# Performance work log

Hardware: AMD Instinct MI355X
Metric: run time of the kernel (lower is better)

The kernel has to match this reference:

```python
import jax, jax.numpy as jnp
import numpy as np

EPS = 1e-06

def phi(x):
    # canonical linear-attention feature map: elu(x) + 1 (positive features)
    return jax.nn.elu(x) + 1.0

def setup_inputs() -> dict:
    key = jax.random.key(0)
    kq, kk, kv = jax.random.split(key, 3)
    B, H, S, D = 4, 16, 4096, 64
    query = jax.random.normal(kq, (B, H, S, D), dtype=jnp.float32)
    k = jax.random.normal(kk, (B, H, S, D), dtype=jnp.float32)
    value = jax.random.normal(kv, (B, H, S, D), dtype=jnp.float32)
    attention_mask = jnp.ones((B, S), dtype=jnp.float32)
    return {"query": query, "key": k, "value": value, "attention_mask": attention_mask}

def reference(query, key, value, attention_mask):
    B, H, S, D = query.shape
    q = query / jnp.sqrt(jnp.asarray(D, query.dtype))
    phi_q = phi(q)                                   # [b,h,n,d]
    phi_k = phi(key)                                 # [b,h,n,d]
    mask = attention_mask[:, None, :, None].astype(phi_k.dtype)  # [b,1,n,1]
    phi_k = phi_k * mask
    kv_term = jnp.einsum('bhnd,bhnv->bhdv', phi_k, value)        # [b,h,d,v]
    output = jnp.einsum('bhnd,bhdv->bhnv', phi_q, kv_term)       # [b,h,n,v]
    k_one = jnp.sum(phi_k, axis=2)                               # [b,h,d] == phi_k @ masked ones
    normalizer = jnp.einsum('bhnd,bhd->bhn', phi_q, k_one)[..., None]  # [b,h,n,1]
    return output / (normalizer + EPS)
```

## Files before the change

### kernel.cpp

```cpp
#include <hip/hip_runtime.h>

typedef unsigned short ushort_t;
typedef unsigned int uint32;
typedef __bf16 bf16x8 __attribute__((ext_vector_type(8)));
typedef float f32x4 __attribute__((ext_vector_type(4)));

#define NB 4
#define NH 16
#define NS 4096
#define ND 64
#define NBH 64
#define EPSF 1e-6f

#define CH1 16
#define ROWS1 (NS / CH1)
#define P2R 64
#define LDJ 70
#define LDJW 35
#define BTSZ (80 * 64)

__device__ __forceinline__ float phi_f(float x) {
    return x > 0.0f ? x + 1.0f : __expf(x);
}
__device__ __forceinline__ ushort_t bf16_rn(float x) {
    uint32 u = __float_as_uint(x);
    uint32 r = (u + 0x7FFFu + ((u >> 16) & 1u)) >> 16;
    return (ushort_t)r;
}
__device__ __forceinline__ void split2(float x, ushort_t& h, ushort_t& l) {
    h = bf16_rn(x);
    float hf = __uint_as_float(((uint32)h) << 16);
    l = bf16_rn(x - hf);
}
union FragU { uint32 u[4]; bf16x8 v; };
__device__ __forceinline__ bf16x8 ld_frag(const ushort_t* arr, int widx) {
    const uint32* p = (const uint32*)arr;
    FragU f;
    f.u[0] = p[widx]; f.u[1] = p[widx + 1]; f.u[2] = p[widx + 2]; f.u[3] = p[widx + 3];
    return f.v;
}
union FragP { ushort_t s[8]; bf16x8 v; };
__device__ __forceinline__ f32x4 mfma16(bf16x8 a, bf16x8 b, f32x4 c) {
    return __builtin_amdgcn_mfma_f32_16x16x32_bf16(a, b, c, 0, 0, 0);
}

template<bool PART>
__global__ __launch_bounds__(256, 4)
void la_pass1(const float* __restrict__ Kin, const float* __restrict__ Vin,
              const float* __restrict__ Min, float* __restrict__ okv,
              float* __restrict__ ok1)
{
    const int t  = threadIdx.x;
    const int cx = blockIdx.x;
    const int bh = blockIdx.y;
    const int bb = bh >> 4;
    const float* Kb = Kin + (long long)bh * NS * ND;
    const float* Vb = Vin + (long long)bh * NS * ND;
    const float* Mb = Min + (long long)bb * NS;

    __shared__ __align__(16) ushort_t skh[64 * LDJ], skl[64 * LDJ];
    __shared__ __align__(16) ushort_t svh[64 * LDJ], svl[64 * LDJ];

    const int rr0 = t >> 4;
    const int c   = (t & 15) * 4;
    const int wv  = t >> 6;
    const int m   = t & 15;
    const int q   = (t & 63) >> 4;

    const f32x4 zf = {0.f, 0.f, 0.f, 0.f};
    f32x4 acc0 = zf, acc1 = zf, acc2 = zf, acc3 = zf;
    float k1loc[4] = {0.f, 0.f, 0.f, 0.f};

    const int s0 = cx * ROWS1;

    float4 kR[2][4], vR[2][4];
    float  mR[2][4];
#define LOADT(tt, sset) { \
        const long long rb_ = (long long)(s0 + (tt) * 64 + rr0); \
        const float* kp_ = Kb + rb_ * ND + c; \
        const float* vp_ = Vb + rb_ * ND + c; \
        kR[sset][0] = *(const float4*)(kp_);            vR[sset][0] = *(const float4*)(vp_); \
        kR[sset][1] = *(const float4*)(kp_ + 16 * ND);  vR[sset][1] = *(const float4*)(vp_ + 16 * ND); \
        kR[sset][2] = *(const float4*)(kp_ + 32 * ND);  vR[sset][2] = *(const float4*)(vp_ + 32 * ND); \
        kR[sset][3] = *(const float4*)(kp_ + 48 * ND);  vR[sset][3] = *(const float4*)(vp_ + 48 * ND); \
        mR[sset][0] = Mb[rb_];      mR[sset][1] = Mb[rb_ + 16]; \
        mR[sset][2] = Mb[rb_ + 32]; mR[sset][3] = Mb[rb_ + 48]; }

    LOADT(0, 0);
    __builtin_amdgcn_sched_barrier(0);

    #pragma unroll
    for (int tile = 0; tile < ROWS1 / 64; ++tile) {
        const int cur = tile & 1;
        const int nxt = cur ^ 1;
        if (tile + 1 < ROWS1 / 64) {
            LOADT(tile + 1, nxt);
            __builtin_amdgcn_sched_barrier(0);
        }
        __syncthreads();
        #pragma unroll
        for (int j = 0; j < 4; ++j) {
            const int rr = rr0 + 16 * j;
            const float xs[4] = {kR[cur][j].x, kR[cur][j].y, kR[cur][j].z, kR[cur][j].w};
            const float vs[4] = {vR[cur][j].x, vR[cur][j].y, vR[cur][j].z, vR[cur][j].w};
            const float mj = mR[cur][j];
            #pragma unroll
            for (int i = 0; i < 4; ++i) {
                const float x = phi_f(xs[i]) * mj;
                k1loc[i] += x;
                ushort_t h, l;
                split2(x, h, l);
                skh[(c + i) * LDJ + rr] = h;
                skl[(c + i) * LDJ + rr] = l;
                split2(vs[i], h, l);
                svh[(c + i) * LDJ + rr] = h;
                svl[(c + i) * LDJ + rr] = l;
            }
        }
        __syncthreads();
        #pragma unroll
        for (int ks = 0; ks < 2; ++ks) {
            const int fo = ks * 16 + q * 4;
            const bf16x8 ah = ld_frag(skh, (16 * wv + m) * LDJW + fo);
            const bf16x8 al = ld_frag(skl, (16 * wv + m) * LDJW + fo);
            {
                const bf16x8 fbh = ld_frag(svh, (0 + m) * LDJW + fo);
                const bf16x8 fbl = ld_frag(svl, (0 + m) * LDJW + fo);
                acc0 = mfma16(al, fbh, acc0); acc0 = mfma16(ah, fbl, acc0); acc0 = mfma16(ah, fbh, acc0);
            }
            {
                const bf16x8 fbh = ld_frag(svh, (16 + m) * LDJW + fo);
                const bf16x8 fbl = ld_frag(svl, (16 + m) * LDJW + fo);
                acc1 = mfma16(al, fbh, acc1); acc1 = mfma16(ah, fbl, acc1); acc1 = mfma16(ah, fbh, acc1);
            }
            {
                const bf16x8 fbh = ld_frag(svh, (32 + m) * LDJW + fo);
                const bf16x8 fbl = ld_frag(svl, (32 + m) * LDJW + fo);
                acc2 = mfma16(al, fbh, acc2); acc2 = mfma16(ah, fbl, acc2); acc2 = mfma16(ah, fbh, acc2);
            }
            {
                const bf16x8 fbh = ld_frag(svh, (48 + m) * LDJW + fo);
                const bf16x8 fbl = ld_frag(svl, (48 + m) * LDJW + fo);
                acc3 = mfma16(al, fbh, acc3); acc3 = mfma16(ah, fbl, acc3); acc3 = mfma16(ah, fbh, acc3);
            }
        }
    }
#undef LOADT

    const int dbase = 16 * wv + q * 4;
    if (PART) {
        float* outp = okv + (long long)(bh * CH1 + cx) * (ND * ND);
        #pragma unroll
        for (int i = 0; i < 4; ++i) {
            outp[(dbase + i) * ND +  0 + m] = acc0[i];
            outp[(dbase + i) * ND + 16 + m] = acc1[i];
            outp[(dbase + i) * ND + 32 + m] = acc2[i];
            outp[(dbase + i) * ND + 48 + m] = acc3[i];
        }
    } else {
        float* outp = okv + (long long)bh * (ND * ND);
        #pragma unroll
        for (int i = 0; i < 4; ++i) {
            atomicAdd(&outp[(dbase + i) * ND +  0 + m], acc0[i]);
            atomicAdd(&outp[(dbase + i) * ND + 16 + m], acc1[i]);
            atomicAdd(&outp[(dbase + i) * ND + 32 + m], acc2[i]);
            atomicAdd(&outp[(dbase + i) * ND + 48 + m], acc3[i]);
        }
    }
    __syncthreads();
    float* red = (float*)skh;
    #pragma unroll
    for (int i = 0; i < 4; ++i) red[(c + i) * 17 + rr0] = k1loc[i];
    __syncthreads();
    if (t < 64) {
        float s = 0.f;
        #pragma unroll
        for (int g = 0; g < 16; ++g) s += red[t * 17 + g];
        if (PART) ok1[(bh * CH1 + cx) * ND + t] = s;
        else      atomicAdd(&ok1[bh * ND + t], s);
    }
}

__global__ __launch_bounds__(256)
void la_reduce(const float* __restrict__ pkv, const float* __restrict__ pk1,
               ushort_t* __restrict__ BTh, ushort_t* __restrict__ BTl)
{
    const int t = threadIdx.x;
    const int bh = blockIdx.x;
    const float4* src = (const float4*)(pkv + (long long)bh * CH1 * ND * ND);
    float4 a[4];
    #pragma unroll
    for (int i = 0; i < 4; ++i) { a[i].x = 0.f; a[i].y = 0.f; a[i].z = 0.f; a[i].w = 0.f; }
    for (int c = 0; c < CH1; ++c) {
        #pragma unroll
        for (int i = 0; i < 4; ++i) {
            const float4 v = src[c * 1024 + t + 256 * i];
            a[i].x += v.x; a[i].y += v.y; a[i].z += v.z; a[i].w += v.w;
        }
    }
    ushort_t* oh = BTh + (long long)bh * BTSZ;
    ushort_t* ol = BTl + (long long)bh * BTSZ;
    #pragma unroll
    for (int i = 0; i < 4; ++i) {
        const int e4 = t + 256 * i;
        const int d  = e4 >> 4;
        const int v0 = (e4 & 15) * 4;
        const float vals[4] = {a[i].x, a[i].y, a[i].z, a[i].w};
        #pragma unroll
        for (int j = 0; j < 4; ++j) {
            ushort_t h, l; split2(vals[j], h, l);
            oh[(v0 + j) * ND + d] = h;
            ol[(v0 + j) * ND + d] = l;
        }
    }
    if (t < ND) {
        float s = 0.f;
        for (int c = 0; c < CH1; ++c) s += pk1[(bh * CH1 + c) * ND + t];
        ushort_t h, l; split2(s, h, l);
        oh[64 * ND + t] = h; ol[64 * ND + t] = l;
    }
    for (int z = t; z < 15 * 64; z += 256) { oh[65 * ND + z] = 0; ol[65 * ND + z] = 0; }
}

__global__ __launch_bounds__(256)
void la_convert(const float* __restrict__ kv, const float* __restrict__ k1,
                ushort_t* __restrict__ BTh, ushort_t* __restrict__ BTl)
{
    const int t = threadIdx.x;
    const int bh = blockIdx.x;
    const float* kvb = kv + (long long)bh * ND * ND;
    ushort_t* oh = BTh + (long long)bh * BTSZ;
    ushort_t* ol = BTl + (long long)bh * BTSZ;
    for (int e = t; e < ND * ND; e += 256) {
        const int d = e >> 6, v = e & 63;
        ushort_t h, l; split2(kvb[e], h, l);
        oh[v * ND + d] = h; ol[v * ND + d] = l;
    }
    if (t < ND) { ushort_t h, l; split2(k1[bh * ND + t], h, l); oh[64 * ND + t] = h; ol[64 * ND + t] = l; }
    for (int z = t; z < 15 * 64; z += 256) { oh[65 * ND + z] = 0; ol[65 * ND + z] = 0; }
}

__global__ __launch_bounds__(256, 2)
void la_pass2(const float* __restrict__ Qin, const ushort_t* __restrict__ BTh,
              const ushort_t* __restrict__ BTl, float* __restrict__ Out)
{
    const int t  = threadIdx.x;
    const int bh = blockIdx.y;
    const int s0 = blockIdx.x * P2R;
    const long long base = (long long)bh * NS * ND;
    const int wv = t >> 6;
    const int m  = t & 15;
    const int q  = (t & 63) >> 4;
    const int lane = t & 63;
    const ushort_t* Bh = BTh + (long long)bh * BTSZ;
    const ushort_t* Bl = BTl + (long long)bh * BTSZ;

    const int row = s0 + 16 * wv + m;
    const float* qp = Qin + base + (long long)row * ND;
    float4 qv[4];
    qv[0] = *(const float4*)(qp + q * 8);
    qv[1] = *(const float4*)(qp + q * 8 + 4);
    qv[2] = *(const float4*)(qp + 32 + q * 8);
    qv[3] = *(const float4*)(qp + 32 + q * 8 + 4);
    bf16x8 fbh[5][2], fbl[5][2];
    #pragma unroll
    for (int nt = 0; nt < 5; ++nt) {
        #pragma unroll
        for (int ks = 0; ks < 2; ++ks) {
            const int bo = (16 * nt + m) * ND + ks * 32 + q * 8;
            fbh[nt][ks] = *(const bf16x8*)(Bh + bo);
            fbl[nt][ks] = *(const bf16x8*)(Bl + bo);
        }
    }
    __builtin_amdgcn_sched_barrier(0);

    bf16x8 aH[2], aL[2];
    #pragma unroll
    for (int ks = 0; ks < 2; ++ks) {
        const float xs[8] = {qv[2 * ks].x, qv[2 * ks].y, qv[2 * ks].z, qv[2 * ks].w,
                             qv[2 * ks + 1].x, qv[2 * ks + 1].y, qv[2 * ks + 1].z, qv[2 * ks + 1].w};
        FragP fh, fl;
        #pragma unroll
        for (int i = 0; i < 8; ++i) {
            ushort_t h, l; split2(phi_f(xs[i] * 0.125f), h, l);
            fh.s[i] = h; fl.s[i] = l;
        }
        aH[ks] = fh.v; aL[ks] = fl.v;
    }

    const f32x4 zf = {0.f, 0.f, 0.f, 0.f};
    f32x4 acc[5];
    #pragma unroll
    for (int b = 0; b < 5; ++b) acc[b] = zf;

    #pragma unroll
    for (int nt = 0; nt < 5; ++nt) {
        #pragma unroll
        for (int ks = 0; ks < 2; ++ks) {
            acc[nt] = mfma16(aL[ks], fbh[nt][ks], acc[nt]);
            acc[nt] = mfma16(aH[ks], fbl[nt][ks], acc[nt]);
            acc[nt] = mfma16(aH[ks], fbh[nt][ks], acc[nt]);
        }
    }

    float* outb = Out + base;
    const int rbase = s0 + 16 * wv + q * 4;
    #pragma unroll
    for (int i = 0; i < 4; ++i) {
        const float nv = __shfl(acc[4][i], lane & 48, 64);
        const float rn = 1.0f / (nv + EPSF);
        const long long ro = (long long)(rbase + i) * ND;
        outb[ro +  0 + m] = acc[0][i] * rn;
        outb[ro + 16 + m] = acc[1][i] * rn;
        outb[ro + 32 + m] = acc[2][i] * rn;
        outb[ro + 48 + m] = acc[3][i] * rn;
    }
}

extern "C" void kernel_launch(void* const* d_in, const int* in_sizes, int n_in,
                              void* d_out, int out_size, void* d_ws, size_t ws_size,
                              hipStream_t stream)
{
    const float* Q = (const float*)d_in[0];
    const float* K = (const float*)d_in[1];
    const float* V = (const float*)d_in[2];
    const float* M = (const float*)d_in[3];
    float* Out = (float*)d_out;

    const size_t partf = (size_t)NBH * CH1 * ND * ND;
    const size_t pk1f  = (size_t)NBH * CH1 * ND;
    const size_t kvf   = (size_t)NBH * ND * ND;
    const size_t k1f   = (size_t)NBH * ND;
    const size_t btu   = (size_t)NBH * BTSZ;
    const size_t need  = (partf + pk1f) * sizeof(float) + 2 * btu * sizeof(ushort_t);

    if (ws_size >= need) {
        float* PKV = (float*)d_ws;
        float* PK1 = PKV + partf;
        ushort_t* BThp = (ushort_t*)(PK1 + pk1f);
        ushort_t* BTlp = BThp + btu;
        la_pass1<true><<<dim3(CH1, NBH), dim3(256), 0, stream>>>(K, V, M, PKV, PK1);
        la_reduce<<<dim3(NBH), dim3(256), 0, stream>>>(PKV, PK1, BThp, BTlp);
        la_pass2<<<dim3(NS / P2R, NBH), dim3(256), 0, stream>>>(Q, BThp, BTlp, Out);
    } else {
        float* KVb = (float*)d_ws;
        float* K1b = KVb + kvf;
        ushort_t* BThp = (ushort_t*)(K1b + k1f);
        ushort_t* BTlp = BThp + btu;
        hipMemsetAsync(d_ws, 0, (kvf + k1f) * sizeof(float), stream);
        la_pass1<false><<<dim3(CH1, NBH), dim3(256), 0, stream>>>(K, V, M, KVb, K1b);
        la_convert<<<dim3(NBH), dim3(256), 0, stream>>>(KVb, K1b, BThp, BTlp);
        la_pass2<<<dim3(NS / P2R, NBH), dim3(256), 0, stream>>>(Q, BThp, BTlp, Out);
    }
}
```

Measured before the change: 272.6 us.

## Process four row tiles per pass2 block and halve pass1 chunking

Pass2 blocks now cover 256 rows instead of 64. Each block loads the bf16 KV fragments once and reuses them across four 64-row sub-tiles, with the Q loads software-pipelined two tiles ahead. Pass1 uses 8 chunks per head instead of 16, which gives longer serial loops and less partial-sum reduction work. The next-tile prefetch in pass1 now issues after the second barrier instead of before the first. Fewer blocks may reduce occupancy and parallelism on the GPU, and the later prefetch may expose more load latency.

```diff
diff --git a/kernel.cpp b/kernel.cpp
--- a/kernel.cpp
+++ b/kernel.cpp
@@ -12,9 +12,9 @@
 #define NBH 64
 #define EPSF 1e-6f
 
-#define CH1 16
+#define CH1 8
 #define ROWS1 (NS / CH1)
-#define P2R 64
+#define NT1 (ROWS1 / 64)
 #define LDJ 70
 #define LDJW 35
 #define BTSZ (80 * 64)
@@ -75,28 +75,22 @@
 
     float4 kR[2][4], vR[2][4];
     float  mR[2][4];
-#define LOADT(tt, sset) { \
+#define LOADT(tt, ss) { \
         const long long rb_ = (long long)(s0 + (tt) * 64 + rr0); \
         const float* kp_ = Kb + rb_ * ND + c; \
         const float* vp_ = Vb + rb_ * ND + c; \
-        kR[sset][0] = *(const float4*)(kp_);            vR[sset][0] = *(const float4*)(vp_); \
-        kR[sset][1] = *(const float4*)(kp_ + 16 * ND);  vR[sset][1] = *(const float4*)(vp_ + 16 * ND); \
-        kR[sset][2] = *(const float4*)(kp_ + 32 * ND);  vR[sset][2] = *(const float4*)(vp_ + 32 * ND); \
-        kR[sset][3] = *(const float4*)(kp_ + 48 * ND);  vR[sset][3] = *(const float4*)(vp_ + 48 * ND); \
-        mR[sset][0] = Mb[rb_];      mR[sset][1] = Mb[rb_ + 16]; \
-        mR[sset][2] = Mb[rb_ + 32]; mR[sset][3] = Mb[rb_ + 48]; }
+        kR[ss][0] = *(const float4*)(kp_);            vR[ss][0] = *(const float4*)(vp_); \
+        kR[ss][1] = *(const float4*)(kp_ + 16 * ND);  vR[ss][1] = *(const float4*)(vp_ + 16 * ND); \
+        kR[ss][2] = *(const float4*)(kp_ + 32 * ND);  vR[ss][2] = *(const float4*)(vp_ + 32 * ND); \
+        kR[ss][3] = *(const float4*)(kp_ + 48 * ND);  vR[ss][3] = *(const float4*)(vp_ + 48 * ND); \
+        mR[ss][0] = Mb[rb_];      mR[ss][1] = Mb[rb_ + 16]; \
+        mR[ss][2] = Mb[rb_ + 32]; mR[ss][3] = Mb[rb_ + 48]; }
 
     LOADT(0, 0);
-    __builtin_amdgcn_sched_barrier(0);
-
-    #pragma unroll
-    for (int tile = 0; tile < ROWS1 / 64; ++tile) {
+
+    #pragma unroll
+    for (int tile = 0; tile < NT1; ++tile) {
         const int cur = tile & 1;
-        const int nxt = cur ^ 1;
-        if (tile + 1 < ROWS1 / 64) {
-            LOADT(tile + 1, nxt);
-            __builtin_amdgcn_sched_barrier(0);
-        }
         __syncthreads();
         #pragma unroll
         for (int j = 0; j < 4; ++j) {
@@ -118,6 +112,9 @@
             }
         }
         __syncthreads();
+        if (tile + 1 < NT1) {
+            LOADT(tile + 1, cur ^ 1);
+        }
         #pragma unroll
         for (int ks = 0; ks < 2; ++ks) {
             const int fo = ks * 16 + q * 4;
@@ -240,45 +237,23 @@
     for (int z = t; z < 15 * 64; z += 256) { oh[65 * ND + z] = 0; ol[65 * ND + z] = 0; }
 }
 
-__global__ __launch_bounds__(256, 2)
-void la_pass2(const float* __restrict__ Qin, const ushort_t* __restrict__ BTh,
-              const ushort_t* __restrict__ BTl, float* __restrict__ Out)
-{
-    const int t  = threadIdx.x;
-    const int bh = blockIdx.y;
-    const int s0 = blockIdx.x * P2R;
-    const long long base = (long long)bh * NS * ND;
-    const int wv = t >> 6;
-    const int m  = t & 15;
-    const int q  = (t & 63) >> 4;
-    const int lane = t & 63;
-    const ushort_t* Bh = BTh + (long long)bh * BTSZ;
-    const ushort_t* Bl = BTl + (long long)bh * BTSZ;
-
-    const int row = s0 + 16 * wv + m;
-    const float* qp = Qin + base + (long long)row * ND;
-    float4 qv[4];
-    qv[0] = *(const float4*)(qp + q * 8);
-    qv[1] = *(const float4*)(qp + q * 8 + 4);
-    qv[2] = *(const float4*)(qp + 32 + q * 8);
-    qv[3] = *(const float4*)(qp + 32 + q * 8 + 4);
-    bf16x8 fbh[5][2], fbl[5][2];
-    #pragma unroll
-    for (int nt = 0; nt < 5; ++nt) {
-        #pragma unroll
-        for (int ks = 0; ks < 2; ++ks) {
-            const int bo = (16 * nt + m) * ND + ks * 32 + q * 8;
-            fbh[nt][ks] = *(const bf16x8*)(Bh + bo);
-            fbl[nt][ks] = *(const bf16x8*)(Bl + bo);
-        }
-    }
-    __builtin_amdgcn_sched_barrier(0);
-
+__device__ __forceinline__ void p2_load(const float* __restrict__ qp, float4* qs, int q)
+{
+    qs[0] = *(const float4*)(qp + q * 8);
+    qs[1] = *(const float4*)(qp + q * 8 + 4);
+    qs[2] = *(const float4*)(qp + 32 + q * 8);
+    qs[3] = *(const float4*)(qp + 32 + q * 8 + 4);
+}
+
+__device__ __forceinline__ void p2_body(const float4* qs, int rbase, int m, int q, int lane,
+                                        const bf16x8 (&fbh)[5][2], const bf16x8 (&fbl)[5][2],
+                                        float* __restrict__ outb)
+{
     bf16x8 aH[2], aL[2];
     #pragma unroll
     for (int ks = 0; ks < 2; ++ks) {
-        const float xs[8] = {qv[2 * ks].x, qv[2 * ks].y, qv[2 * ks].z, qv[2 * ks].w,
-                             qv[2 * ks + 1].x, qv[2 * ks + 1].y, qv[2 * ks + 1].z, qv[2 * ks + 1].w};
+        const float xs[8] = {qs[2 * ks].x, qs[2 * ks].y, qs[2 * ks].z, qs[2 * ks].w,
+                             qs[2 * ks + 1].x, qs[2 * ks + 1].y, qs[2 * ks + 1].z, qs[2 * ks + 1].w};
         FragP fh, fl;
         #pragma unroll
         for (int i = 0; i < 8; ++i) {
@@ -287,12 +262,10 @@
         }
         aH[ks] = fh.v; aL[ks] = fl.v;
     }
-
     const f32x4 zf = {0.f, 0.f, 0.f, 0.f};
     f32x4 acc[5];
     #pragma unroll
     for (int b = 0; b < 5; ++b) acc[b] = zf;
-
     #pragma unroll
     for (int nt = 0; nt < 5; ++nt) {
         #pragma unroll
@@ -302,9 +275,6 @@
             acc[nt] = mfma16(aH[ks], fbh[nt][ks], acc[nt]);
         }
     }
-
-    float* outb = Out + base;
-    const int rbase = s0 + 16 * wv + q * 4;
     #pragma unroll
     for (int i = 0; i < 4; ++i) {
         const float nv = __shfl(acc[4][i], lane & 48, 64);
@@ -317,6 +287,53 @@
     }
 }
 
+__global__ __launch_bounds__(256, 2)
+void la_pass2(const float* __restrict__ Qin, const ushort_t* __restrict__ BTh,
+              const ushort_t* __restrict__ BTl, float* __restrict__ Out)
+{
+    const int t  = threadIdx.x;
+    const int bh = blockIdx.y;
+    const int s0 = blockIdx.x * 256;
+    const long long base = (long long)bh * NS * ND;
+    const int wv = t >> 6;
+    const int m  = t & 15;
+    const int q  = (t & 63) >> 4;
+    const int lane = t & 63;
+    const ushort_t* Bh = BTh + (long long)bh * BTSZ;
+    const ushort_t* Bl = BTl + (long long)bh * BTSZ;
+    float* outb = Out + base;
+
+    bf16x8 fbh[5][2], fbl[5][2];
+    #pragma unroll
+    for (int nt = 0; nt < 5; ++nt) {
+        #pragma unroll
+        for (int ks = 0; ks < 2; ++ks) {
+            const int bo = (16 * nt + m) * ND + ks * 32 + q * 8;
+            fbh[nt][ks] = *(const bf16x8*)(Bh + bo);
+            fbl[nt][ks] = *(const bf16x8*)(Bl + bo);
+        }
+    }
+
+    const float* qp0 = Qin + base + (long long)(s0 + (0 * 4 + wv) * 16 + m) * ND;
+    const float* qp1 = Qin + base + (long long)(s0 + (1 * 4 + wv) * 16 + m) * ND;
+    const float* qp2 = Qin + base + (long long)(s0 + (2 * 4 + wv) * 16 + m) * ND;
+    const float* qp3 = Qin + base + (long long)(s0 + (3 * 4 + wv) * 16 + m) * ND;
+    const int rb0 = s0 + (0 * 4 + wv) * 16 + q * 4;
+    const int rb1 = s0 + (1 * 4 + wv) * 16 + q * 4;
+    const int rb2 = s0 + (2 * 4 + wv) * 16 + q * 4;
+    const int rb3 = s0 + (3 * 4 + wv) * 16 + q * 4;
+
+    float4 qA[4], qB[4];
+    p2_load(qp0, qA, q);
+    p2_load(qp1, qB, q);
+    p2_body(qA, rb0, m, q, lane, fbh, fbl, outb);
+    p2_load(qp2, qA, q);
+    p2_body(qB, rb1, m, q, lane, fbh, fbl, outb);
+    p2_load(qp3, qB, q);
+    p2_body(qA, rb2, m, q, lane, fbh, fbl, outb);
+    p2_body(qB, rb3, m, q, lane, fbh, fbl, outb);
+}
+
 extern "C" void kernel_launch(void* const* d_in, const int* in_sizes, int n_in,
                               void* d_out, int out_size, void* d_ws, size_t ws_size,
                               hipStream_t stream)
@@ -341,7 +358,7 @@
         ushort_t* BTlp = BThp + btu;
         la_pass1<true><<<dim3(CH1, NBH), dim3(256), 0, stream>>>(K, V, M, PKV, PK1);
         la_reduce<<<dim3(NBH), dim3(256), 0, stream>>>(PKV, PK1, BThp, BTlp);
-        la_pass2<<<dim3(NS / P2R, NBH), dim3(256), 0, stream>>>(Q, BThp, BTlp, Out);
+        la_pass2<<<dim3(NS / 256, NBH), dim3(256), 0, stream>>>(Q, BThp, BTlp, Out);
     } else {
         float* KVb = (float*)d_ws;
         float* K1b = KVb + kvf;
@@ -350,6 +367,6 @@
         hipMemsetAsync(d_ws, 0, (kvf + k1f) * sizeof(float), stream);
         la_pass1<false><<<dim3(CH1, NBH), dim3(256), 0, stream>>>(K, V, M, KVb, K1b);
         la_convert<<<dim3(NBH), dim3(256), 0, stream>>>(KVb, K1b, BThp, BTlp);
-        la_pass2<<<dim3(NS / P2R, NBH), dim3(256), 0, stream>>>(Q, BThp, BTlp, Out);
-    }
-}
+        la_pass2<<<dim3(NS / 256, NBH), dim3(256), 0, stream>>>(Q, BThp, BTlp, Out);
+    }
+}
```

New measurement: 248.8 us. 1.1x faster.
